# Kernel tuning notes

Measured on AMD Instinct MI355X. Metric: run time of the kernel, lower is better.

## Reference

```python
import jax, jax.numpy as jnp
import numpy as np

N_STU, N_ITEM, N_CONC = 10000, 50000, 2048
EDGES, K = 250000, 4
EMB, CNUM = 64, 128


def setup_inputs() -> dict:
    key = jax.random.key(0)
    ks = jax.random.split(key, 10)
    return {
        "stu_idx": jax.random.randint(ks[0], (EDGES,), 0, N_STU),
        "item_idx": jax.random.randint(ks[1], (EDGES,), 0, N_ITEM),
        "conc_idx": jax.random.randint(ks[2], (EDGES, K), 0, N_CONC),
        "stu_fusion": jax.random.normal(ks[3], (N_STU, EMB), jnp.float32),
        "item_fusion": jax.random.normal(ks[4], (N_ITEM, EMB), jnp.float32),
        "concept_fusion": jax.random.normal(ks[5], (N_CONC, EMB), jnp.float32),
        # factor weights are non-negative in the original (NoneNegClipper)
        "W_stu": jax.random.uniform(ks[6], (CNUM, 2 * EMB), jnp.float32) * 0.1,
        "W_item": jax.random.uniform(ks[7], (CNUM, 2 * EMB), jnp.float32) * 0.1,
        "w_pred": jax.random.uniform(ks[8], (CNUM,), jnp.float32) * 0.1,
        "b_pred": jax.random.normal(ks[9], (1,), jnp.float32),
    }


def reference(stu_idx, item_idx, conc_idx, stu_fusion, item_fusion,
              concept_fusion, W_stu, W_item, w_pred, b_pred):
    emb = stu_fusion.shape[1]
    # split Linear(2*emb -> CNUM) into the two cat halves: out = x1 @ Wa.T + x2 @ Wb.T
    Ws_a, Ws_b = W_stu[:, :emb], W_stu[:, emb:]
    Wi_a, Wi_b = W_item[:, :emb], W_item[:, emb:]

    # per-entity projections computed once on the tables, then gathered (cheap)
    stu_part = (stu_fusion @ Ws_a.T)[stu_idx]      # [E, CNUM]
    item_part = (item_fusion @ Wi_a.T)[item_idx]   # [E, CNUM]
    conc_stu = (concept_fusion @ Ws_b.T)[conc_idx]   # [E, K, CNUM]
    conc_item = (concept_fusion @ Wi_b.T)[conc_idx]  # [E, K, CNUM]

    stu_out = jax.nn.sigmoid(stu_part[:, None, :] + conc_stu)    # [E, K, CNUM]
    item_out = jax.nn.sigmoid(item_part[:, None, :] + conc_item)  # [E, K, CNUM]
    diff = stu_out - item_out
    per_conc = jax.nn.sigmoid(jnp.einsum('ekc,c->ek', diff, w_pred) + b_pred[0])  # [E, K]
    return per_conc.mean(axis=1)  # [E]
```

## Files before the change

### kernel.cpp

```cpp
#include <hip/hip_runtime.h>
#include <hip/hip_bf16.h>
#include <hip/hip_fp16.h>

constexpr int EDGES = 250000;
constexpr int EMB   = 64;
constexpr int CNUM  = 128;
constexpr int NSTU  = 10000;
constexpr int NITEM = 50000;
constexpr int NCONC = 2048;

constexpr size_t ESP_OFF = 0;
constexpr size_t EIP_OFF = ESP_OFF + (size_t)NSTU  * CNUM;
constexpr size_t ECS_OFF = EIP_OFF + (size_t)NITEM * CNUM;
constexpr size_t ECI_OFF = ECS_OFF + (size_t)NCONC * CNUM;
constexpr size_t WH_OFF  = ECI_OFF + (size_t)NCONC * CNUM;

constexpr float NEG_LOG2E = -1.44269504088896340736f;

constexpr int STU_JOBS  = NSTU  / 16;
constexpr int ITEM_JOBS = NITEM / 16;
constexpr int CONC_JOBS = (NCONC / 16) * 2;
constexpr int NJOBS     = STU_JOBS + ITEM_JOBS + CONC_JOBS;
constexpr int PROJ_BLKS = (NJOBS + 3) / 4;

typedef _Float16 h8 __attribute__((ext_vector_type(8)));
typedef _Float16 h4 __attribute__((ext_vector_type(4)));
typedef _Float16 h2 __attribute__((ext_vector_type(2)));
typedef float    f32x4 __attribute__((ext_vector_type(4)));

__device__ __forceinline__ h8 pack8(float4 lo, float4 hi) {
    h8 h;
    h[0] = (_Float16)lo.x; h[1] = (_Float16)lo.y;
    h[2] = (_Float16)lo.z; h[3] = (_Float16)lo.w;
    h[4] = (_Float16)hi.x; h[5] = (_Float16)hi.y;
    h[6] = (_Float16)hi.z; h[7] = (_Float16)hi.w;
    return h;
}

__device__ __forceinline__ _Float16 rcp16(_Float16 x) {
#if __has_builtin(__builtin_amdgcn_rcph)
    return __builtin_amdgcn_rcph(x);
#else
    return (_Float16)__builtin_amdgcn_rcpf((float)x);
#endif
}

template <int CTRL>
__device__ __forceinline__ float dppadd(float x) {
    return x + __int_as_float(__builtin_amdgcn_update_dpp(
        0, __float_as_int(x), CTRL, 0xf, 0xf, true));
}

__global__ __launch_bounds__(256) void proj_mfma(
        const float* __restrict__ stuF, const float* __restrict__ itemF,
        const float* __restrict__ concF,
        const float* __restrict__ W_stu, const float* __restrict__ W_item,
        const float* __restrict__ w_pred,
        _Float16* __restrict__ ESP, _Float16* __restrict__ EIP,
        _Float16* __restrict__ ECS, _Float16* __restrict__ ECI,
        _Float16* __restrict__ WH) {
    const int tid  = threadIdx.x;
    const int lane = tid & 63;
    const int job  = blockIdx.x * 4 + (tid >> 6);
    if (job >= NJOBS) return;

    if (job == 0) {
        const float2 wv2 = ((const float2*)w_pred)[lane];
        h2 wh; wh[0] = (_Float16)wv2.x; wh[1] = (_Float16)wv2.y;
        *(h2*)(WH + 2 * lane) = wh;
    }

    const float* F; const float* W; _Float16* O; int strip, wcol;
    if (job < STU_JOBS) {
        F = stuF;  W = W_stu;  O = ESP; strip = job; wcol = 0;
    } else if (job < STU_JOBS + ITEM_JOBS) {
        F = itemF; W = W_item; O = EIP; strip = job - STU_JOBS; wcol = 0;
    } else {
        const int g = job - STU_JOBS - ITEM_JOBS;
        F = concF; W = (g & 1) ? W_item : W_stu; O = (g & 1) ? ECI : ECS;
        strip = g >> 1; wcol = EMB;
    }

    const int m = lane & 15;
    const int q = lane >> 4;
    const int row = strip * 16 + m;

    const float4* fa = (const float4*)(F + (size_t)row * EMB + q * 8);
    const float4* fb = (const float4*)(F + (size_t)row * EMB + 32 + q * 8);
    const h8 A0 = pack8(fa[0], fa[1]);
    const h8 A1 = pack8(fb[0], fb[1]);

    const int orow = strip * 16 + q * 4;

#pragma unroll
    for (int ct = 0; ct < 8; ++ct) {
        const int ch = ct * 16 + m;
        const float* wr = W + (size_t)ch * (2 * EMB) + wcol;
        const float4* wb0 = (const float4*)(wr + q * 8);
        const float4* wb1 = (const float4*)(wr + 32 + q * 8);
        const h8 B0 = pack8(wb0[0], wb0[1]);
        const h8 B1 = pack8(wb1[0], wb1[1]);

        f32x4 acc = {0.f, 0.f, 0.f, 0.f};
        acc = __builtin_amdgcn_mfma_f32_16x16x32_f16(A0, B0, acc, 0, 0, 0);
        acc = __builtin_amdgcn_mfma_f32_16x16x32_f16(A1, B1, acc, 0, 0, 0);

#pragma unroll
        for (int r = 0; r < 4; ++r) {
            const float e = __builtin_amdgcn_exp2f(acc[r] * NEG_LOG2E);
            O[(size_t)(orow + r) * CNUM + ct * 16 + m] = (_Float16)e;
        }
    }
}

__device__ __forceinline__ float sigm(float x) {
    return __builtin_amdgcn_rcpf(1.f + __builtin_amdgcn_exp2f(x * NEG_LOG2E));
}

__global__ __launch_bounds__(256) void edge_kernel(
        const int*  __restrict__ stu_idx,
        const int*  __restrict__ item_idx,
        const int4* __restrict__ conc_idx,
        const _Float16* __restrict__ ESP,
        const _Float16* __restrict__ EIP,
        const _Float16* __restrict__ ECS,
        const _Float16* __restrict__ ECI,
        const _Float16* __restrict__ WH,
        const float* __restrict__ b_pred,
        float* __restrict__ out) {
    const int lane = threadIdx.x & 63;
    const int wvg  = (blockIdx.x * blockDim.x + threadIdx.x) >> 6;
    const int sub  = lane >> 4;
    const int li   = lane & 15;
    const int e    = wvg * 4 + sub;

    const int s  = stu_idx[e];
    const int it = item_idx[e];
    const int4 c4 = conc_idx[e];

    const h8 es = *(const h8*)(ESP + (size_t)s  * CNUM + li * 8);
    const h8 ei = *(const h8*)(EIP + (size_t)it * CNUM + li * 8);
    const h8 w8 = *(const h8*)(WH + li * 8);
    const float b = b_pred[0];

    const h8 ONE = {(_Float16)1, (_Float16)1, (_Float16)1, (_Float16)1,
                    (_Float16)1, (_Float16)1, (_Float16)1, (_Float16)1};

    const int ck[4] = {c4.x, c4.y, c4.z, c4.w};
    float p[4];
#pragma unroll
    for (int k = 0; k < 4; ++k) {
        const h8 cs = *(const h8*)(ECS + (size_t)ck[k] * CNUM + li * 8);
        const h8 ci = *(const h8*)(ECI + (size_t)ck[k] * CNUM + li * 8);
        const h8 t   = es * cs;
        const h8 u   = ei * ci;
        const h8 den = (t + ONE) * (u + ONE);
        const h8 num = w8 * (u - t);
        h8 r;
#pragma unroll
        for (int i = 0; i < 8; ++i) r[i] = num[i] * rcp16(den[i]);
        const h4 q4 = __builtin_shufflevector(r, r, 0, 1, 2, 3)
                    + __builtin_shufflevector(r, r, 4, 5, 6, 7);
        const h2 q2 = __builtin_shufflevector(q4, q4, 0, 1)
                    + __builtin_shufflevector(q4, q4, 2, 3);
        p[k] = (float)q2[0] + (float)q2[1];
    }

#pragma unroll
    for (int j = 0; j < 4; ++j) p[j] = dppadd<0xB1>(p[j]);
#pragma unroll
    for (int j = 0; j < 4; ++j) p[j] = dppadd<0x4E>(p[j]);
#pragma unroll
    for (int j = 0; j < 4; ++j) p[j] = dppadd<0x141>(p[j]);
#pragma unroll
    for (int j = 0; j < 4; ++j) p[j] = dppadd<0x140>(p[j]);

    const float r = 0.25f * (sigm(p[0] + b) + sigm(p[1] + b) +
                             sigm(p[2] + b) + sigm(p[3] + b));
    if (li == 0) out[e] = r;
}

extern "C" void kernel_launch(void* const* d_in, const int* in_sizes, int n_in,
                              void* d_out, int out_size, void* d_ws, size_t ws_size,
                              hipStream_t stream) {
    const int* stu_idx  = (const int*)d_in[0];
    const int* item_idx = (const int*)d_in[1];
    const int* conc_idx = (const int*)d_in[2];
    const float* stu_fusion     = (const float*)d_in[3];
    const float* item_fusion    = (const float*)d_in[4];
    const float* concept_fusion = (const float*)d_in[5];
    const float* W_stu          = (const float*)d_in[6];
    const float* W_item         = (const float*)d_in[7];
    const float* w_pred         = (const float*)d_in[8];
    const float* b_pred         = (const float*)d_in[9];
    float* out = (float*)d_out;

    _Float16* ESP = (_Float16*)d_ws + ESP_OFF;
    _Float16* EIP = (_Float16*)d_ws + EIP_OFF;
    _Float16* ECS = (_Float16*)d_ws + ECS_OFF;
    _Float16* ECI = (_Float16*)d_ws + ECI_OFF;
    _Float16* WH  = (_Float16*)d_ws + WH_OFF;

    proj_mfma<<<PROJ_BLKS, 256, 0, stream>>>(
        stu_fusion, item_fusion, concept_fusion, W_stu, W_item, w_pred,
        ESP, EIP, ECS, ECI, WH);

    edge_kernel<<<EDGES / 16, 256, 0, stream>>>(
        stu_idx, item_idx, (const int4*)conc_idx,
        ESP, EIP, ECS, ECI, WH, b_pred, out);
}
```

Measured before the change: 136.2 us.

## Convert edge kernel to persistent grid-stride loop with software-pipelined gathers

The edge kernel now launches a fixed 1024 blocks, and each wavefront loops over groups of four edges. Index loads and row gathers for later groups are issued before the current group's compute, with two register sets alternating. The goal is to hide gather latency through explicit prefetch instead of relying on many short-lived waves. The cost is higher register pressure and fewer resident waves, and clamped indices cause some redundant loads past the end.

```diff
diff --git a/kernel.cpp b/kernel.cpp
--- a/kernel.cpp
+++ b/kernel.cpp
@@ -22,6 +22,10 @@
 constexpr int CONC_JOBS = (NCONC / 16) * 2;
 constexpr int NJOBS     = STU_JOBS + ITEM_JOBS + CONC_JOBS;
 constexpr int PROJ_BLKS = (NJOBS + 3) / 4;
+
+constexpr int NGROUPS    = EDGES / 4;
+constexpr int EDGE_BLKS  = 1024;
+constexpr int NW         = EDGE_BLKS * 4;
 
 typedef _Float16 h8 __attribute__((ext_vector_type(8)));
 typedef _Float16 h4 __attribute__((ext_vector_type(4)));
@@ -117,6 +121,79 @@
     return __builtin_amdgcn_rcpf(1.f + __builtin_amdgcn_exp2f(x * NEG_LOG2E));
 }
 
+struct EIdx { int s, it; int4 c; };
+struct ERows { h8 es, ei, cs0, ci0, cs1, ci1, cs2, ci2, cs3, ci3; };
+
+__device__ __forceinline__ EIdx load_idx(
+        int g, int sub,
+        const int* __restrict__ stu_idx, const int* __restrict__ item_idx,
+        const int4* __restrict__ conc_idx) {
+    const int e = min(g, NGROUPS - 1) * 4 + sub;
+    EIdx x;
+    x.s  = stu_idx[e];
+    x.it = item_idx[e];
+    x.c  = conc_idx[e];
+    return x;
+}
+
+__device__ __forceinline__ ERows load_rows(
+        const EIdx& x, int li,
+        const _Float16* __restrict__ ESP, const _Float16* __restrict__ EIP,
+        const _Float16* __restrict__ ECS, const _Float16* __restrict__ ECI) {
+    ERows r;
+    r.es  = *(const h8*)(ESP + (size_t)x.s   * CNUM + li * 8);
+    r.ei  = *(const h8*)(EIP + (size_t)x.it  * CNUM + li * 8);
+    r.cs0 = *(const h8*)(ECS + (size_t)x.c.x * CNUM + li * 8);
+    r.ci0 = *(const h8*)(ECI + (size_t)x.c.x * CNUM + li * 8);
+    r.cs1 = *(const h8*)(ECS + (size_t)x.c.y * CNUM + li * 8);
+    r.ci1 = *(const h8*)(ECI + (size_t)x.c.y * CNUM + li * 8);
+    r.cs2 = *(const h8*)(ECS + (size_t)x.c.z * CNUM + li * 8);
+    r.ci2 = *(const h8*)(ECI + (size_t)x.c.z * CNUM + li * 8);
+    r.cs3 = *(const h8*)(ECS + (size_t)x.c.w * CNUM + li * 8);
+    r.ci3 = *(const h8*)(ECI + (size_t)x.c.w * CNUM + li * 8);
+    return r;
+}
+
+__device__ __forceinline__ float chan8(const h8 es, const h8 ei,
+                                       const h8 cs, const h8 ci,
+                                       const h8 w8, const h8 ONE) {
+    const h8 t   = es * cs;
+    const h8 u   = ei * ci;
+    const h8 den = (t + ONE) * (u + ONE);
+    const h8 num = w8 * (u - t);
+    h8 r;
+#pragma unroll
+    for (int i = 0; i < 8; ++i) r[i] = num[i] * rcp16(den[i]);
+    const h4 q4 = __builtin_shufflevector(r, r, 0, 1, 2, 3)
+                + __builtin_shufflevector(r, r, 4, 5, 6, 7);
+    const h2 q2 = __builtin_shufflevector(q4, q4, 0, 1)
+                + __builtin_shufflevector(q4, q4, 2, 3);
+    return (float)q2[0] + (float)q2[1];
+}
+
+__device__ __forceinline__ void compute_store(
+        const ERows& r, int g, int sub, int li,
+        const h8 w8, const h8 ONE, float b, float* __restrict__ out) {
+    float p[4];
+    p[0] = chan8(r.es, r.ei, r.cs0, r.ci0, w8, ONE);
+    p[1] = chan8(r.es, r.ei, r.cs1, r.ci1, w8, ONE);
+    p[2] = chan8(r.es, r.ei, r.cs2, r.ci2, w8, ONE);
+    p[3] = chan8(r.es, r.ei, r.cs3, r.ci3, w8, ONE);
+
+#pragma unroll
+    for (int j = 0; j < 4; ++j) p[j] = dppadd<0xB1>(p[j]);
+#pragma unroll
+    for (int j = 0; j < 4; ++j) p[j] = dppadd<0x4E>(p[j]);
+#pragma unroll
+    for (int j = 0; j < 4; ++j) p[j] = dppadd<0x141>(p[j]);
+#pragma unroll
+    for (int j = 0; j < 4; ++j) p[j] = dppadd<0x140>(p[j]);
+
+    const float res = 0.25f * (sigm(p[0] + b) + sigm(p[1] + b) +
+                               sigm(p[2] + b) + sigm(p[3] + b));
+    if (li == 0) out[g * 4 + sub] = res;
+}
+
 __global__ __launch_bounds__(256) void edge_kernel(
         const int*  __restrict__ stu_idx,
         const int*  __restrict__ item_idx,
@@ -129,55 +206,30 @@
         const float* __restrict__ b_pred,
         float* __restrict__ out) {
     const int lane = threadIdx.x & 63;
-    const int wvg  = (blockIdx.x * blockDim.x + threadIdx.x) >> 6;
+    const int wid  = (blockIdx.x * blockDim.x + threadIdx.x) >> 6;
     const int sub  = lane >> 4;
     const int li   = lane & 15;
-    const int e    = wvg * 4 + sub;
-
-    const int s  = stu_idx[e];
-    const int it = item_idx[e];
-    const int4 c4 = conc_idx[e];
-
-    const h8 es = *(const h8*)(ESP + (size_t)s  * CNUM + li * 8);
-    const h8 ei = *(const h8*)(EIP + (size_t)it * CNUM + li * 8);
+
     const h8 w8 = *(const h8*)(WH + li * 8);
     const float b = b_pred[0];
-
     const h8 ONE = {(_Float16)1, (_Float16)1, (_Float16)1, (_Float16)1,
                     (_Float16)1, (_Float16)1, (_Float16)1, (_Float16)1};
 
-    const int ck[4] = {c4.x, c4.y, c4.z, c4.w};
-    float p[4];
-#pragma unroll
-    for (int k = 0; k < 4; ++k) {
-        const h8 cs = *(const h8*)(ECS + (size_t)ck[k] * CNUM + li * 8);
-        const h8 ci = *(const h8*)(ECI + (size_t)ck[k] * CNUM + li * 8);
-        const h8 t   = es * cs;
-        const h8 u   = ei * ci;
-        const h8 den = (t + ONE) * (u + ONE);
-        const h8 num = w8 * (u - t);
-        h8 r;
-#pragma unroll
-        for (int i = 0; i < 8; ++i) r[i] = num[i] * rcp16(den[i]);
-        const h4 q4 = __builtin_shufflevector(r, r, 0, 1, 2, 3)
-                    + __builtin_shufflevector(r, r, 4, 5, 6, 7);
-        const h2 q2 = __builtin_shufflevector(q4, q4, 0, 1)
-                    + __builtin_shufflevector(q4, q4, 2, 3);
-        p[k] = (float)q2[0] + (float)q2[1];
-    }
-
-#pragma unroll
-    for (int j = 0; j < 4; ++j) p[j] = dppadd<0xB1>(p[j]);
-#pragma unroll
-    for (int j = 0; j < 4; ++j) p[j] = dppadd<0x4E>(p[j]);
-#pragma unroll
-    for (int j = 0; j < 4; ++j) p[j] = dppadd<0x141>(p[j]);
-#pragma unroll
-    for (int j = 0; j < 4; ++j) p[j] = dppadd<0x140>(p[j]);
-
-    const float r = 0.25f * (sigm(p[0] + b) + sigm(p[1] + b) +
-                             sigm(p[2] + b) + sigm(p[3] + b));
-    if (li == 0) out[e] = r;
+    int g = wid;
+    EIdx  ia = load_idx(g, sub, stu_idx, item_idx, conc_idx);
+    ERows ra = load_rows(ia, li, ESP, EIP, ECS, ECI);
+    EIdx  ib = load_idx(g + NW, sub, stu_idx, item_idx, conc_idx);
+
+    for (; g < NGROUPS; g += 2 * NW) {
+        ERows rb = load_rows(ib, li, ESP, EIP, ECS, ECI);
+        ia = load_idx(g + 2 * NW, sub, stu_idx, item_idx, conc_idx);
+        compute_store(ra, g, sub, li, w8, ONE, b, out);
+
+        ra = load_rows(ia, li, ESP, EIP, ECS, ECI);
+        ib = load_idx(g + 3 * NW, sub, stu_idx, item_idx, conc_idx);
+        if (g + NW < NGROUPS)
+            compute_store(rb, g + NW, sub, li, w8, ONE, b, out);
+    }
 }
 
 extern "C" void kernel_launch(void* const* d_in, const int* in_sizes, int n_in,
@@ -205,7 +257,7 @@
         stu_fusion, item_fusion, concept_fusion, W_stu, W_item, w_pred,
         ESP, EIP, ECS, ECI, WH);
 
-    edge_kernel<<<EDGES / 16, 256, 0, stream>>>(
+    edge_kernel<<<EDGE_BLKS, 256, 0, stream>>>(
         stu_idx, item_idx, (const int4*)conc_idx,
         ESP, EIP, ECS, ECI, WH, b_pred, out);
 }
```

New measurement: 143.6 us. 1.05x slower.
